# Optimization experiments

Hardware: AMD Instinct MI355X
Metric: run time of the kernel (lower is better)

Reference implementation:

```python
import jax, jax.numpy as jnp
import numpy as np

DECAY = 0.99
EPS = 1e-06


def setup_inputs() -> dict:
    key = jax.random.key(0)
    k1, k2, k3 = jax.random.split(key, 3)
    B, S, D, K = 8, 8192, 256, 2048
    x = jax.random.normal(k1, (B, S, D), dtype=jnp.float32)
    embed = jax.random.normal(k2, (K, D), dtype=jnp.float32)
    cluster_size = jnp.ones((K,), dtype=jnp.float32)
    embed_avg = jax.random.normal(k3, (K, D), dtype=jnp.float32)
    return {"x": x, "embed": embed, "cluster_size": cluster_size, "embed_avg": embed_avg}


def reference(x, embed, cluster_size, embed_avg):
    # x: [B, S, D]; embed/embed_avg: [K, D]; cluster_size: [K]
    B, S, D = x.shape
    K = embed.shape[0]
    xf = x.reshape(-1, D)  # [N, D]
    dist = (
        jnp.sum(xf * xf, axis=1, keepdims=True)
        - 2.0 * (xf @ embed.T)
        + jnp.sum(embed * embed, axis=1)
    )
    embed_ind_flat = jnp.argmin(dist, axis=-1)  # [N]
    quantize = embed[embed_ind_flat].reshape(B, S, D)
    embed_ind = embed_ind_flat.reshape(B, S)

    # EMA updates (training branch). one_hot.sum(0) == per-code counts,
    # one_hot.T @ x == per-code feature sums; use segment_sum (no NxK one-hot).
    counts = jax.ops.segment_sum(
        jnp.ones((B * S,), dtype=jnp.float32), embed_ind_flat, num_segments=K
    )
    embed_sum = jax.ops.segment_sum(xf, embed_ind_flat, num_segments=K)  # [K, D]
    new_cluster_size = cluster_size * DECAY + (1.0 - DECAY) * counts
    new_embed_avg = embed_avg * DECAY + (1.0 - DECAY) * embed_sum
    total = new_cluster_size.sum()
    smoothed = (new_cluster_size + EPS) / (total + EPS * K) * total  # laplace smoothing
    new_embed = new_embed_avg / smoothed[:, None]
    return quantize, embed_ind, new_cluster_size, new_embed_avg, new_embed
```

## Files before the change

kernel.cpp:

```cpp
#include <hip/hip_runtime.h>
#include <hip/hip_bf16.h>
#include <float.h>

#define DECAY 0.99f
#define OMD   0.01f
#define EPSF  1e-6f

constexpr int Bb = 8, Ss = 8192, Dd = 256, Kk = 2048;
constexpr int Nn = Bb * Ss;

constexpr long OUT_QUANT = 0;
constexpr long OUT_IND   = (long)Nn * Dd;
constexpr long OUT_NCS   = OUT_IND + Nn;
constexpr long OUT_NEA   = OUT_NCS + Kk;
constexpr long OUT_NE    = OUT_NEA + (long)Kk * Dd;

constexpr long WS_COUNTS = 0;
constexpr long WS_TOTAL  = 2048;
constexpr long WS_EE     = 2112;
constexpr long WS_BIG    = 4160;
constexpr int  PARTS     = 8;
constexpr int  CODES     = 8;

typedef __attribute__((ext_vector_type(8))) short short8;
typedef __attribute__((ext_vector_type(4))) float floatx4;

#define WINDOW 0.0625f

__device__ __forceinline__ void gl_lds(const ushort* g, ushort* l)
{
    __builtin_amdgcn_global_load_lds(
        (const __attribute__((address_space(1))) void*)g,
        (__attribute__((address_space(3))) void*)l,
        16, 0, 0);
}

__global__ __launch_bounds__(256) void convert_x_kernel(
    const float* __restrict__ x, ushort* __restrict__ x_hi, ushort* __restrict__ x_lo)
{
    long base = ((long)blockIdx.x * 256 + threadIdx.x) * 4;
    float4 v = *(const float4*)&x[base];
    float vv[4] = {v.x, v.y, v.z, v.w};
    ushort hh[4], ll[4];
    #pragma unroll
    for (int i = 0; i < 4; ++i) {
        __hip_bfloat16 hb = __float2bfloat16(vv[i]);
        float r = vv[i] - __bfloat162float(hb);
        __hip_bfloat16 lb = __float2bfloat16(r);
        hh[i] = *(ushort*)&hb; ll[i] = *(ushort*)&lb;
    }
    ushort4 h; h.x = hh[0]; h.y = hh[1]; h.z = hh[2]; h.w = hh[3];
    ushort4 l; l.x = ll[0]; l.y = ll[1]; l.z = ll[2]; l.w = ll[3];
    *(ushort4*)&x_hi[base] = h;
    *(ushort4*)&x_lo[base] = l;
}

__global__ __launch_bounds__(256) void convert_e_kernel(
    const float* __restrict__ embed, ushort* __restrict__ e_hi,
    ushort* __restrict__ e_lo, float* __restrict__ ee)
{
    int row  = blockIdx.x * 4 + (threadIdx.x >> 6);
    int lane = threadIdx.x & 63;
    long base = (long)row * Dd + lane * 4;
    float4 v = *(const float4*)&embed[base];
    float vv[4] = {v.x, v.y, v.z, v.w};
    ushort hh[4], ll[4];
    float s = 0.0f;
    #pragma unroll
    for (int i = 0; i < 4; ++i) {
        s += vv[i] * vv[i];
        __hip_bfloat16 hb = __float2bfloat16(vv[i]);
        float r = vv[i] - __bfloat162float(hb);
        __hip_bfloat16 lb = __float2bfloat16(r);
        hh[i] = *(ushort*)&hb; ll[i] = *(ushort*)&lb;
    }
    ushort4 h; h.x = hh[0]; h.y = hh[1]; h.z = hh[2]; h.w = hh[3];
    ushort4 l; l.x = ll[0]; l.y = ll[1]; l.z = ll[2]; l.w = ll[3];
    *(ushort4*)&e_hi[base] = h;
    *(ushort4*)&e_lo[base] = l;
    #pragma unroll
    for (int off = 32; off >= 1; off >>= 1)
        s += __shfl_xor(s, off, 64);
    if (lane == 0) ee[row] = s;
}

__global__ __attribute__((amdgpu_waves_per_eu(2, 2))) __launch_bounds__(256)
void pass1_kernel(
    const ushort* __restrict__ x_hi, const ushort* __restrict__ x_lo,
    const ushort* __restrict__ e_hi, const ushort* __restrict__ e_lo,
    const float* __restrict__ ee, float* __restrict__ ind_out,
    int* __restrict__ qbase)
{
    __shared__ __attribute__((aligned(16))) ushort ah[128 * 32];
    __shared__ __attribute__((aligned(16))) ushort al[128 * 32];
    __shared__ __attribute__((aligned(16))) ushort bh[256 * 32];
    __shared__ __attribute__((aligned(16))) ushort bl[256 * 32];
    __shared__ float  redv[2][128];
    __shared__ float  red2[2][128];
    __shared__ int    redi[2][128];

    const int tid  = threadIdx.x;
    const int lane = tid & 63;
    const int quad = lane >> 4;
    const int l15  = lane & 15;
    const int w    = tid >> 6;
    const int wy   = w >> 1;
    const int wx   = w & 1;
    const long row0 = (long)blockIdx.x * 128;

    const int rloc   = lane >> 2;
    const int cchunk = (lane & 3) ^ ((rloc >> 1) & 3);
    const int gcoff  = rloc * 256 + cchunk * 8;

    const int sread = (l15 >> 1) & 3;
    const int aoff0 = ((wy * 64 + l15) << 5) + ((quad ^ sread) << 3);
    const int boff0 = ((wx * 128 + l15) << 5) + ((quad ^ sread) << 3);

    float bestv[16], best2v[16];
    int   besti[16];
    #pragma unroll
    for (int i = 0; i < 16; ++i) { bestv[i] = FLT_MAX; best2v[i] = FLT_MAX; besti[i] = 0; }

    for (int ct = 0; ct < Kk / 256; ++ct) {
        floatx4 acc[4][8];
        #pragma unroll
        for (int rt = 0; rt < 4; ++rt)
            #pragma unroll
            for (int jt = 0; jt < 8; ++jt)
                acc[rt][jt] = (floatx4){0.f, 0.f, 0.f, 0.f};

        const long brow = (long)ct * 256;

        for (int kc = 0; kc < 8; ++kc) {
            const int kcol = kc * 32;

            __syncthreads();
            gl_lds(&x_hi[((row0 + w * 16) << 8) + kcol + gcoff],       &ah[w * 512]);
            gl_lds(&x_hi[((row0 + (w + 4) * 16) << 8) + kcol + gcoff], &ah[(w + 4) * 512]);
            gl_lds(&x_lo[((row0 + w * 16) << 8) + kcol + gcoff],       &al[w * 512]);
            gl_lds(&x_lo[((row0 + (w + 4) * 16) << 8) + kcol + gcoff], &al[(w + 4) * 512]);
            #pragma unroll
            for (int i = 0; i < 4; ++i) {
                const int seg = w + 4 * i;
                gl_lds(&e_hi[((brow + seg * 16) << 8) + kcol + gcoff], &bh[seg * 512]);
                gl_lds(&e_lo[((brow + seg * 16) << 8) + kcol + gcoff], &bl[seg * 512]);
            }
            __syncthreads();

            short8 afh[4], afl[4];
            #pragma unroll
            for (int rt = 0; rt < 4; ++rt)
                afh[rt] = *(const short8*)&ah[aoff0 + (rt << 9)];
            #pragma unroll
            for (int rt = 0; rt < 4; ++rt)
                afl[rt] = *(const short8*)&al[aoff0 + (rt << 9)];

            #pragma unroll
            for (int jt = 0; jt < 8; ++jt) {
                short8 bfh = *(const short8*)&bh[boff0 + (jt << 9)];
                short8 bfl = *(const short8*)&bl[boff0 + (jt << 9)];
                #pragma unroll
                for (int rt = 0; rt < 4; ++rt)
                    acc[rt][jt] = __builtin_amdgcn_mfma_f32_16x16x32_bf16(
                        afh[rt], bfh, acc[rt][jt], 0, 0, 0);
                #pragma unroll
                for (int rt = 0; rt < 4; ++rt)
                    acc[rt][jt] = __builtin_amdgcn_mfma_f32_16x16x32_bf16(
                        afl[rt], bfh, acc[rt][jt], 0, 0, 0);
                #pragma unroll
                for (int rt = 0; rt < 4; ++rt)
                    acc[rt][jt] = __builtin_amdgcn_mfma_f32_16x16x32_bf16(
                        afh[rt], bfl, acc[rt][jt], 0, 0, 0);
            }
        }

        #pragma unroll
        for (int jt = 0; jt < 8; ++jt) {
            int c = ct * 256 + wx * 128 + jt * 16 + l15;
            float eec = ee[c];
            #pragma unroll
            for (int rt = 0; rt < 4; ++rt) {
                #pragma unroll
                for (int reg = 0; reg < 4; ++reg) {
                    float s = eec - 2.0f * acc[rt][jt][reg];
                    int slot = rt * 4 + reg;
                    if (s < bestv[slot]) {
                        best2v[slot] = bestv[slot];
                        bestv[slot] = s; besti[slot] = c;
                    } else {
                        best2v[slot] = fminf(best2v[slot], s);
                    }
                }
            }
        }
    }

    #pragma unroll
    for (int slot = 0; slot < 16; ++slot) {
        float bv = bestv[slot]; int bi = besti[slot]; float b2 = best2v[slot];
        #pragma unroll
        for (int off = 8; off >= 1; off >>= 1) {
            float ov  = __shfl_xor(bv, off, 16);
            int   oi  = __shfl_xor(bi, off, 16);
            float ov2 = __shfl_xor(b2, off, 16);
            float nm2 = fminf(fminf(b2, ov2), fmaxf(bv, ov));
            if (ov < bv) { bv = ov; bi = oi; }
            b2 = nm2;
        }
        bestv[slot] = bv; besti[slot] = bi; best2v[slot] = b2;
    }

    if (l15 == 0) {
        #pragma unroll
        for (int rt = 0; rt < 4; ++rt)
            #pragma unroll
            for (int reg = 0; reg < 4; ++reg) {
                int rloc2 = wy * 64 + rt * 16 + quad * 4 + reg;
                int slot = rt * 4 + reg;
                redv[wx][rloc2] = bestv[slot];
                red2[wx][rloc2] = best2v[slot];
                redi[wx][rloc2] = besti[slot];
            }
    }
    __syncthreads();
    if (tid < 128) {
        float v0 = redv[0][tid], v1 = redv[1][tid];
        float s0 = red2[0][tid], s1 = red2[1][tid];
        float m1, m2; int mi;
        if (v0 <= v1) { m1 = v0; mi = redi[0][tid]; m2 = fminf(fminf(s0, s1), v1); }
        else          { m1 = v1; mi = redi[1][tid]; m2 = fminf(fminf(s0, s1), v0); }
        long rowAbs = row0 + tid;
        ind_out[rowAbs] = (float)mi;
        if (m2 - m1 <= WINDOW) {
            int q = atomicAdd(qbase, 1);
            qbase[1 + q] = (int)rowAbs;
        }
    }
}

constexpr int RB = 8;
__global__ __launch_bounds__(256) void pass2_kernel(
    const float* __restrict__ x, const float* __restrict__ embed,
    const float* __restrict__ ee, const int* __restrict__ qbase,
    float* __restrict__ ind_out)
{
    __shared__ float xs[RB][256];
    __shared__ float sv[RB][256];
    __shared__ int   si[RB][256];
    const int tid = threadIdx.x;
    const int count = qbase[0];

    for (int q0 = blockIdx.x * RB; q0 < count; q0 += gridDim.x * RB) {
        const int nr = (count - q0 < RB) ? (count - q0) : RB;
        __syncthreads();
        for (int r = 0; r < nr; ++r)
            xs[r][tid] = x[(long)qbase[1 + q0 + r] * Dd + tid];
        __syncthreads();

        float bv[RB]; int bi[RB];
        #pragma unroll
        for (int r = 0; r < RB; ++r) { bv[r] = FLT_MAX; bi[r] = 0; }

        for (int i = 0; i < Kk / 256; ++i) {
            const int c = i * 256 + tid;
            const float4* er = (const float4*)&embed[(long)c * Dd];
            float dot[RB];
            #pragma unroll
            for (int r = 0; r < RB; ++r) dot[r] = 0.0f;
            for (int d = 0; d < Dd / 4; ++d) {
                float4 e4 = er[d];
                #pragma unroll
                for (int r = 0; r < RB; ++r) {
                    float4 x4 = *(const float4*)&xs[r][d * 4];
                    dot[r] += e4.x * x4.x + e4.y * x4.y + e4.z * x4.z + e4.w * x4.w;
                }
            }
            float eec = ee[c];
            #pragma unroll
            for (int r = 0; r < RB; ++r) {
                float s = eec - 2.0f * dot[r];
                if (s < bv[r]) { bv[r] = s; bi[r] = c; }
            }
        }

        #pragma unroll
        for (int r = 0; r < RB; ++r) { sv[r][tid] = bv[r]; si[r][tid] = bi[r]; }
        __syncthreads();
        for (int off = 128; off >= 1; off >>= 1) {
            if (tid < off) {
                #pragma unroll
                for (int r = 0; r < RB; ++r) {
                    float v2 = sv[r][tid + off]; int i2 = si[r][tid + off];
                    if (v2 < sv[r][tid] || (v2 == sv[r][tid] && i2 < si[r][tid])) {
                        sv[r][tid] = v2; si[r][tid] = i2;
                    }
                }
            }
            __syncthreads();
        }
        if (tid < nr)
            ind_out[qbase[1 + q0 + tid]] = (float)si[tid][0];
        __syncthreads();
    }
}

__global__ __launch_bounds__(256) void quant_gather_kernel(
    const float* __restrict__ embed, const float* __restrict__ ind_f,
    float* __restrict__ quant)
{
    long row  = (long)blockIdx.x * 4 + (threadIdx.x >> 6);
    int  lane = threadIdx.x & 63;
    int  idx  = (int)ind_f[row];
    float4 ev = *(const float4*)&embed[(long)idx * Dd + lane * 4];
    *(float4*)&quant[row * Dd + lane * 4] = ev;
}

template <int USE_ATOMIC>
__global__ __launch_bounds__(256) void segsum_kernel(
    const float* __restrict__ x, const float* __restrict__ ind_f,
    float* __restrict__ dst, float* __restrict__ counts)
{
    __shared__ float part[CODES][4][256];
    __shared__ float cnt_l[CODES][4];
    const int tid  = threadIdx.x;
    const int w    = tid >> 6;
    const int lane = tid & 63;
    const int k0   = (blockIdx.x >> 3) * CODES;
    const int s    = blockIdx.x & 7;

    constexpr int STRIP = Nn / PARTS;
    constexpr int WAVE_ROWS = STRIP / 4;
    const int base0 = s * STRIP + w * WAVE_ROWS;

    float4 acc[CODES];
    int    cnt[CODES];
    #pragma unroll
    for (int c = 0; c < CODES; ++c) { acc[c] = (float4){0.f,0.f,0.f,0.f}; cnt[c] = 0; }

    for (int win = 0; win < WAVE_ROWS; win += 64) {
        int idx = (int)ind_f[base0 + win + lane];
        unsigned rel = (unsigned)(idx - k0);
        unsigned long long m = __ballot(rel < (unsigned)CODES);
        while (m) {
            int l = __ffsll((unsigned long long)m) - 1;
            m &= m - 1;
            int code = __shfl((int)rel, l, 64);
            long row = base0 + win + l;
            float4 v = *(const float4*)&x[row * Dd + lane * 4];
            switch (code) {
                case 0: acc[0].x+=v.x; acc[0].y+=v.y; acc[0].z+=v.z; acc[0].w+=v.w; cnt[0]++; break;
                case 1: acc[1].x+=v.x; acc[1].y+=v.y; acc[1].z+=v.z; acc[1].w+=v.w; cnt[1]++; break;
                case 2: acc[2].x+=v.x; acc[2].y+=v.y; acc[2].z+=v.z; acc[2].w+=v.w; cnt[2]++; break;
                case 3: acc[3].x+=v.x; acc[3].y+=v.y; acc[3].z+=v.z; acc[3].w+=v.w; cnt[3]++; break;
                case 4: acc[4].x+=v.x; acc[4].y+=v.y; acc[4].z+=v.z; acc[4].w+=v.w; cnt[4]++; break;
                case 5: acc[5].x+=v.x; acc[5].y+=v.y; acc[5].z+=v.z; acc[5].w+=v.w; cnt[5]++; break;
                case 6: acc[6].x+=v.x; acc[6].y+=v.y; acc[6].z+=v.z; acc[6].w+=v.w; cnt[6]++; break;
                case 7: acc[7].x+=v.x; acc[7].y+=v.y; acc[7].z+=v.z; acc[7].w+=v.w; cnt[7]++; break;
            }
        }
    }

    #pragma unroll
    for (int c = 0; c < CODES; ++c) {
        *(float4*)&part[c][w][lane * 4] = acc[c];
        if (lane == 0) cnt_l[c][w] = (float)cnt[c];
    }
    __syncthreads();

    #pragma unroll
    for (int c = 0; c < CODES; ++c) {
        float sum = part[c][0][tid] + part[c][1][tid] + part[c][2][tid] + part[c][3][tid];
        if (USE_ATOMIC) {
            if (sum != 0.0f) atomicAdd(&dst[(long)(k0 + c) * Dd + tid], sum);
        } else {
            dst[((long)s * Kk + (k0 + c)) * Dd + tid] = sum;
        }
    }
    if (tid < CODES)
        atomicAdd(&counts[k0 + tid],
                  cnt_l[tid][0] + cnt_l[tid][1] + cnt_l[tid][2] + cnt_l[tid][3]);
}

__global__ __launch_bounds__(256) void ema_cs_kernel(
    const float* __restrict__ cs, const float* __restrict__ counts,
    float* __restrict__ ncs, float* __restrict__ total_ws)
{
    __shared__ float red[256];
    int tid = threadIdx.x;
    float s = 0.0f;
    #pragma unroll
    for (int i = 0; i < 8; ++i) {
        int k = tid + i * 256;
        float v = cs[k] * DECAY + OMD * counts[k];
        ncs[k] = v;
        s += v;
    }
    red[tid] = s;
    __syncthreads();
    #pragma unroll
    for (int off = 128; off >= 1; off >>= 1) {
        if (tid < off) red[tid] += red[tid + off];
        __syncthreads();
    }
    if (tid == 0) total_ws[0] = red[0];
}

__global__ __launch_bounds__(256) void nea_ne_kernel(
    const float* __restrict__ ea, const float* __restrict__ partials,
    int nparts, const float* __restrict__ ncs, const float* __restrict__ total_ws,
    float* __restrict__ nea, float* __restrict__ ne)
{
    long g = ((long)blockIdx.x * 256 + threadIdx.x) * 4;
    int  k = (int)(g >> 8);
    int  d = (int)(g & 255);

    float4 sv = {0.f, 0.f, 0.f, 0.f};
    for (int p = 0; p < nparts; ++p) {
        float4 pv = *(const float4*)&partials[((long)p * Kk + k) * Dd + d];
        sv.x += pv.x; sv.y += pv.y; sv.z += pv.z; sv.w += pv.w;
    }

    float4 av = *(const float4*)&ea[g];
    float4 out_nea;
    out_nea.x = av.x * DECAY + OMD * sv.x;
    out_nea.y = av.y * DECAY + OMD * sv.y;
    out_nea.z = av.z * DECAY + OMD * sv.z;
    out_nea.w = av.w * DECAY + OMD * sv.w;
    *(float4*)&nea[g] = out_nea;

    float total = total_ws[0];
    float sm = (ncs[k] + EPSF) / (total + EPSF * (float)Kk) * total;
    float inv = 1.0f / sm;
    float4 out_ne;
    out_ne.x = out_nea.x * inv;
    out_ne.y = out_nea.y * inv;
    out_ne.z = out_nea.z * inv;
    out_ne.w = out_nea.w * inv;
    *(float4*)&ne[g] = out_ne;
}

extern "C" void kernel_launch(void* const* d_in, const int* in_sizes, int n_in,
                              void* d_out, int out_size, void* d_ws, size_t ws_size,
                              hipStream_t stream)
{
    const float* x     = (const float*)d_in[0];
    const float* embed = (const float*)d_in[1];
    const float* cs    = (const float*)d_in[2];
    const float* ea    = (const float*)d_in[3];

    float* out   = (float*)d_out;
    float* quant = out + OUT_QUANT;
    float* ind_f = out + OUT_IND;
    float* ncs   = out + OUT_NCS;
    float* nea   = out + OUT_NEA;
    float* ne    = out + OUT_NE;

    float* ws     = (float*)d_ws;
    float* counts = ws + WS_COUNTS;
    float* total  = ws + WS_TOTAL;
    float* ee     = ws + WS_EE;
    float* big    = ws + WS_BIG;

    ushort* x_hi = (ushort*)(out + OUT_QUANT);
    ushort* x_lo = (ushort*)(out + OUT_QUANT + Nn * (Dd / 2));
    ushort* e_hi = (ushort*)(out + OUT_NEA);
    ushort* e_lo = (ushort*)(out + OUT_NEA + Kk * (Dd / 2));
    int*    qb   = (int*)(out + OUT_NE);

    const size_t need_partials =
        (size_t)(WS_BIG + (long)PARTS * Kk * Dd) * sizeof(float) + 1024;
    const bool use_ws_partials = ws_size >= need_partials;

    hipMemsetAsync(counts, 0, Kk * sizeof(float), stream);
    hipMemsetAsync(qb, 0, sizeof(int), stream);
    if (!use_ws_partials)
        hipMemsetAsync(big, 0, (size_t)Kk * Dd * sizeof(float), stream);

    convert_x_kernel<<<(Nn * Dd / 4) / 256, 256, 0, stream>>>(x, x_hi, x_lo);
    convert_e_kernel<<<Kk / 4, 256, 0, stream>>>(embed, e_hi, e_lo, ee);
    pass1_kernel<<<Nn / 128, 256, 0, stream>>>(x_hi, x_lo, e_hi, e_lo, ee, ind_f, qb);
    pass2_kernel<<<256, 256, 0, stream>>>(x, embed, ee, qb, ind_f);
    quant_gather_kernel<<<Nn / 4, 256, 0, stream>>>(embed, ind_f, quant);
    if (use_ws_partials)
        segsum_kernel<0><<<(Kk / CODES) * PARTS, 256, 0, stream>>>(x, ind_f, big, counts);
    else
        segsum_kernel<1><<<(Kk / CODES) * PARTS, 256, 0, stream>>>(x, ind_f, big, counts);
    ema_cs_kernel<<<1, 256, 0, stream>>>(cs, counts, ncs, total);
    nea_ne_kernel<<<(Kk * Dd / 4) / 256, 256, 0, stream>>>(
        ea, big, use_ws_partials ? PARTS : 1, ncs, total, nea, ne);
}
```

Baseline: 487.6 us.

## Replace split-bf16 triple MFMA with single fp16 MFMA and wider refine window

The distance GEMM in pass1 moves from a three-product bf16 hi/lo split to a single fp16 MFMA per tile. K-chunks widen to 64 with a new XOR swizzle, and the lo-part buffers are dropped. This cuts matrix work to a third and halves operand traffic. The lower precision is offset by widening the near-tie window that sends rows to the exact fp32 refine pass, and pass2 gets twice as many blocks to absorb the larger candidate count.

```diff
diff --git a/kernel.cpp b/kernel.cpp
--- a/kernel.cpp
+++ b/kernel.cpp
@@ -1,5 +1,5 @@
 #include <hip/hip_runtime.h>
-#include <hip/hip_bf16.h>
+#include <hip/hip_fp16.h>
 #include <float.h>
 
 #define DECAY 0.99f
@@ -23,9 +23,10 @@
 constexpr int  CODES     = 8;
 
 typedef __attribute__((ext_vector_type(8))) short short8;
+typedef __attribute__((ext_vector_type(8))) _Float16 half8;
 typedef __attribute__((ext_vector_type(4))) float floatx4;
 
-#define WINDOW 0.0625f
+#define WINDOW 0.5f
 
 __device__ __forceinline__ void gl_lds(const ushort* g, ushort* l)
 {
@@ -35,49 +36,38 @@
         16, 0, 0);
 }
 
+__device__ __forceinline__ ushort f2h(float v)
+{
+    __half h = __float2half(v);
+    return *(ushort*)&h;
+}
+
 __global__ __launch_bounds__(256) void convert_x_kernel(
-    const float* __restrict__ x, ushort* __restrict__ x_hi, ushort* __restrict__ x_lo)
-{
-    long base = ((long)blockIdx.x * 256 + threadIdx.x) * 4;
-    float4 v = *(const float4*)&x[base];
-    float vv[4] = {v.x, v.y, v.z, v.w};
-    ushort hh[4], ll[4];
-    #pragma unroll
-    for (int i = 0; i < 4; ++i) {
-        __hip_bfloat16 hb = __float2bfloat16(vv[i]);
-        float r = vv[i] - __bfloat162float(hb);
-        __hip_bfloat16 lb = __float2bfloat16(r);
-        hh[i] = *(ushort*)&hb; ll[i] = *(ushort*)&lb;
-    }
-    ushort4 h; h.x = hh[0]; h.y = hh[1]; h.z = hh[2]; h.w = hh[3];
-    ushort4 l; l.x = ll[0]; l.y = ll[1]; l.z = ll[2]; l.w = ll[3];
-    *(ushort4*)&x_hi[base] = h;
-    *(ushort4*)&x_lo[base] = l;
+    const float* __restrict__ x, ushort* __restrict__ x_h)
+{
+    long base = ((long)blockIdx.x * 256 + threadIdx.x) * 8;
+    float4 a = *(const float4*)&x[base];
+    float4 b = *(const float4*)&x[base + 4];
+    short8 h;
+    h[0] = (short)f2h(a.x); h[1] = (short)f2h(a.y);
+    h[2] = (short)f2h(a.z); h[3] = (short)f2h(a.w);
+    h[4] = (short)f2h(b.x); h[5] = (short)f2h(b.y);
+    h[6] = (short)f2h(b.z); h[7] = (short)f2h(b.w);
+    *(short8*)&x_h[base] = h;
 }
 
 __global__ __launch_bounds__(256) void convert_e_kernel(
-    const float* __restrict__ embed, ushort* __restrict__ e_hi,
-    ushort* __restrict__ e_lo, float* __restrict__ ee)
+    const float* __restrict__ embed, ushort* __restrict__ e_h,
+    float* __restrict__ ee)
 {
     int row  = blockIdx.x * 4 + (threadIdx.x >> 6);
     int lane = threadIdx.x & 63;
     long base = (long)row * Dd + lane * 4;
     float4 v = *(const float4*)&embed[base];
-    float vv[4] = {v.x, v.y, v.z, v.w};
-    ushort hh[4], ll[4];
-    float s = 0.0f;
-    #pragma unroll
-    for (int i = 0; i < 4; ++i) {
-        s += vv[i] * vv[i];
-        __hip_bfloat16 hb = __float2bfloat16(vv[i]);
-        float r = vv[i] - __bfloat162float(hb);
-        __hip_bfloat16 lb = __float2bfloat16(r);
-        hh[i] = *(ushort*)&hb; ll[i] = *(ushort*)&lb;
-    }
-    ushort4 h; h.x = hh[0]; h.y = hh[1]; h.z = hh[2]; h.w = hh[3];
-    ushort4 l; l.x = ll[0]; l.y = ll[1]; l.z = ll[2]; l.w = ll[3];
-    *(ushort4*)&e_hi[base] = h;
-    *(ushort4*)&e_lo[base] = l;
+    float s = v.x * v.x + v.y * v.y + v.z * v.z + v.w * v.w;
+    ushort4 h;
+    h.x = f2h(v.x); h.y = f2h(v.y); h.z = f2h(v.z); h.w = f2h(v.w);
+    *(ushort4*)&e_h[base] = h;
     #pragma unroll
     for (int off = 32; off >= 1; off >>= 1)
         s += __shfl_xor(s, off, 64);
@@ -86,15 +76,12 @@
 
 __global__ __attribute__((amdgpu_waves_per_eu(2, 2))) __launch_bounds__(256)
 void pass1_kernel(
-    const ushort* __restrict__ x_hi, const ushort* __restrict__ x_lo,
-    const ushort* __restrict__ e_hi, const ushort* __restrict__ e_lo,
+    const ushort* __restrict__ x_h, const ushort* __restrict__ e_h,
     const float* __restrict__ ee, float* __restrict__ ind_out,
     int* __restrict__ qbase)
 {
-    __shared__ __attribute__((aligned(16))) ushort ah[128 * 32];
-    __shared__ __attribute__((aligned(16))) ushort al[128 * 32];
-    __shared__ __attribute__((aligned(16))) ushort bh[256 * 32];
-    __shared__ __attribute__((aligned(16))) ushort bl[256 * 32];
+    __shared__ __attribute__((aligned(16))) ushort ah[128 * 64];
+    __shared__ __attribute__((aligned(16))) ushort bh[256 * 64];
     __shared__ float  redv[2][128];
     __shared__ float  red2[2][128];
     __shared__ int    redi[2][128];
@@ -108,13 +95,11 @@
     const int wx   = w & 1;
     const long row0 = (long)blockIdx.x * 128;
 
-    const int rloc   = lane >> 2;
-    const int cchunk = (lane & 3) ^ ((rloc >> 1) & 3);
+    const int rloc   = lane >> 3;
+    const int cchunk = (lane & 7) ^ rloc;
     const int gcoff  = rloc * 256 + cchunk * 8;
 
-    const int sread = (l15 >> 1) & 3;
-    const int aoff0 = ((wy * 64 + l15) << 5) + ((quad ^ sread) << 3);
-    const int boff0 = ((wx * 128 + l15) << 5) + ((quad ^ sread) << 3);
+    const int s7 = l15 & 7;
 
     float bestv[16], best2v[16];
     int   besti[16];
@@ -131,46 +116,37 @@
 
         const long brow = (long)ct * 256;
 
-        for (int kc = 0; kc < 8; ++kc) {
-            const int kcol = kc * 32;
+        for (int kc = 0; kc < 4; ++kc) {
+            const int kcol = kc * 64;
 
             __syncthreads();
-            gl_lds(&x_hi[((row0 + w * 16) << 8) + kcol + gcoff],       &ah[w * 512]);
-            gl_lds(&x_hi[((row0 + (w + 4) * 16) << 8) + kcol + gcoff], &ah[(w + 4) * 512]);
-            gl_lds(&x_lo[((row0 + w * 16) << 8) + kcol + gcoff],       &al[w * 512]);
-            gl_lds(&x_lo[((row0 + (w + 4) * 16) << 8) + kcol + gcoff], &al[(w + 4) * 512]);
             #pragma unroll
             for (int i = 0; i < 4; ++i) {
-                const int seg = w + 4 * i;
-                gl_lds(&e_hi[((brow + seg * 16) << 8) + kcol + gcoff], &bh[seg * 512]);
-                gl_lds(&e_lo[((brow + seg * 16) << 8) + kcol + gcoff], &bl[seg * 512]);
+                const int u = w + 4 * i;
+                gl_lds(&x_h[((row0 + u * 8) << 8) + kcol + gcoff], &ah[u * 512]);
+            }
+            #pragma unroll
+            for (int i = 0; i < 8; ++i) {
+                const int u = w + 4 * i;
+                gl_lds(&e_h[((brow + u * 8) << 8) + kcol + gcoff], &bh[u * 512]);
             }
             __syncthreads();
 
-            short8 afh[4], afl[4];
-            #pragma unroll
-            for (int rt = 0; rt < 4; ++rt)
-                afh[rt] = *(const short8*)&ah[aoff0 + (rt << 9)];
-            #pragma unroll
-            for (int rt = 0; rt < 4; ++rt)
-                afl[rt] = *(const short8*)&al[aoff0 + (rt << 9)];
-
-            #pragma unroll
-            for (int jt = 0; jt < 8; ++jt) {
-                short8 bfh = *(const short8*)&bh[boff0 + (jt << 9)];
-                short8 bfl = *(const short8*)&bl[boff0 + (jt << 9)];
+            #pragma unroll
+            for (int ks = 0; ks < 2; ++ks) {
+                const int cterm = (((ks * 4 + quad) ^ s7) * 8);
+                half8 af[4];
                 #pragma unroll
                 for (int rt = 0; rt < 4; ++rt)
-                    acc[rt][jt] = __builtin_amdgcn_mfma_f32_16x16x32_bf16(
-                        afh[rt], bfh, acc[rt][jt], 0, 0, 0);
+                    af[rt] = *(const half8*)&ah[((wy * 64 + rt * 16 + l15) << 6) + cterm];
                 #pragma unroll
-                for (int rt = 0; rt < 4; ++rt)
-                    acc[rt][jt] = __builtin_amdgcn_mfma_f32_16x16x32_bf16(
-                        afl[rt], bfh, acc[rt][jt], 0, 0, 0);
-                #pragma unroll
-                for (int rt = 0; rt < 4; ++rt)
-                    acc[rt][jt] = __builtin_amdgcn_mfma_f32_16x16x32_bf16(
-                        afh[rt], bfl, acc[rt][jt], 0, 0, 0);
+                for (int jt = 0; jt < 8; ++jt) {
+                    half8 bf = *(const half8*)&bh[((wx * 128 + jt * 16 + l15) << 6) + cterm];
+                    #pragma unroll
+                    for (int rt = 0; rt < 4; ++rt)
+                        acc[rt][jt] = __builtin_amdgcn_mfma_f32_16x16x32_f16(
+                            af[rt], bf, acc[rt][jt], 0, 0, 0);
+                }
             }
         }
 
@@ -461,11 +437,9 @@
     float* ee     = ws + WS_EE;
     float* big    = ws + WS_BIG;
 
-    ushort* x_hi = (ushort*)(out + OUT_QUANT);
-    ushort* x_lo = (ushort*)(out + OUT_QUANT + Nn * (Dd / 2));
-    ushort* e_hi = (ushort*)(out + OUT_NEA);
-    ushort* e_lo = (ushort*)(out + OUT_NEA + Kk * (Dd / 2));
-    int*    qb   = (int*)(out + OUT_NE);
+    ushort* x_h = (ushort*)(out + OUT_QUANT);
+    ushort* e_h = (ushort*)(out + OUT_NEA);
+    int*    qb  = (int*)(out + OUT_NE);
 
     const size_t need_partials =
         (size_t)(WS_BIG + (long)PARTS * Kk * Dd) * sizeof(float) + 1024;
@@ -476,10 +450,10 @@
     if (!use_ws_partials)
         hipMemsetAsync(big, 0, (size_t)Kk * Dd * sizeof(float), stream);
 
-    convert_x_kernel<<<(Nn * Dd / 4) / 256, 256, 0, stream>>>(x, x_hi, x_lo);
-    convert_e_kernel<<<Kk / 4, 256, 0, stream>>>(embed, e_hi, e_lo, ee);
-    pass1_kernel<<<Nn / 128, 256, 0, stream>>>(x_hi, x_lo, e_hi, e_lo, ee, ind_f, qb);
-    pass2_kernel<<<256, 256, 0, stream>>>(x, embed, ee, qb, ind_f);
+    convert_x_kernel<<<(Nn * Dd / 8) / 256, 256, 0, stream>>>(x, x_h);
+    convert_e_kernel<<<Kk / 4, 256, 0, stream>>>(embed, e_h, ee);
+    pass1_kernel<<<Nn / 128, 256, 0, stream>>>(x_h, e_h, ee, ind_f, qb);
+    pass2_kernel<<<512, 256, 0, stream>>>(x, embed, ee, qb, ind_f);
     quant_gather_kernel<<<Nn / 4, 256, 0, stream>>>(embed, ind_f, quant);
     if (use_ws_partials)
         segsum_kernel<0><<<(Kk / CODES) * PARTS, 256, 0, stream>>>(x, ind_f, big, counts);
```

Measured after the change: 478.9 us. About the same (-1.8%).
